# Kernel optimization log

Hardware: AMD Instinct MI355X
Metric: run time of the kernel (lower is better)

Reference implementation:

```python
import jax, jax.numpy as jnp
import numpy as np

TOP_K = 2

def setup_inputs() -> dict:
    key = jax.random.key(0)
    k0, k1, k2, k3 = jax.random.split(key, 4)
    B, S, D, F, E = 4, 4096, 1024, 2048, 8
    x = jax.random.normal(k0, (B, S, D), dtype=jnp.float32)
    w_router = jax.random.normal(k1, (E, D), dtype=jnp.float32) * 0.02
    w1 = jax.random.normal(k2, (E, F, D), dtype=jnp.float32) * 0.02
    w2 = jax.random.normal(k3, (E, D, F), dtype=jnp.float32) * 0.02
    return {"x": x, "w_router": w_router, "w1": w1, "w2": w2}

def reference(x, w_router, w1, w2):
    # x: [B,S,D]; w_router: [E,D]; w1: [E,F,D]; w2: [E,D,F]
    B, S, D = x.shape
    E = w_router.shape[0]
    xf = x.reshape(-1, D)                      # [T,D], T = B*S
    T = xf.shape[0]
    logits = xf @ w_router.T                   # [T,E]
    probs = jax.nn.softmax(logits, axis=-1)    # [T,E]
    top_v, top_i = jax.lax.top_k(probs, TOP_K) # [T,K]
    top_v = top_v / jnp.sum(top_v, axis=-1, keepdims=True)
    # dense combine weights: w[t,e] = renormalized prob if e in top-k else 0
    comb = jnp.zeros_like(probs).at[jnp.arange(T)[:, None], top_i].add(top_v)  # [T,E]
    # dense per-expert compute, masked/weighted combine (same math as gather-MLP-scatter;
    # dropout is identity in eval). GELU is exact (erf), matching torch F.gelu default.
    out = jnp.zeros_like(xf)
    for e in range(E):  # small fixed expert loop
        h = jax.nn.gelu(xf @ w1[e].T, approximate=False)   # [T,F]
        out = out + comb[:, e:e + 1] * (h @ w2[e].T)       # [T,D]
    expert_usage = jnp.mean(probs, axis=0)                  # [E]
    aux_loss = E * jnp.sum(expert_usage ** 2)
    return out.reshape(B, S, D), aux_loss
```

## Files before the change

### kernel.cpp

```cpp
#include <hip/hip_runtime.h>
#include <hip/hip_bf16.h>
#include <math.h>

typedef __attribute__((ext_vector_type(8))) short s16x8;
typedef __attribute__((ext_vector_type(4))) float f32x4;

#define T_TOK 16384
#define D_DIM 1024
#define F_DIM 2048
#define E_NUM 8
#define RCAP 34816

__device__ __forceinline__ unsigned short f2b(float f) {
  unsigned u = __float_as_uint(f);
  u += 0x7fff + ((u >> 16) & 1);
  return (unsigned short)(u >> 16);
}
__device__ __forceinline__ unsigned pk2(float a, float b) {
  __hip_bfloat162 h = __float22bfloat162_rn(make_float2(a, b));
  return *reinterpret_cast<unsigned*>(&h);
}

__global__ void castw_k(const float* __restrict__ w1, const float* __restrict__ w2,
                        unsigned short* __restrict__ w1b, unsigned short* __restrict__ w2b) {
  size_t i = ((size_t)blockIdx.x * 256 + threadIdx.x) * 4;
  float4 a = *(const float4*)(w1 + i);
  float4 b = *(const float4*)(w2 + i);
  uint2 ua, ub;
  ua.x = pk2(a.x, a.y); ua.y = pk2(a.z, a.w);
  ub.x = pk2(b.x, b.y); ub.y = pk2(b.z, b.w);
  *(uint2*)(w1b + i) = ua;
  *(uint2*)(w2b + i) = ub;
}

__global__ void router_k(const float* __restrict__ x, const float* __restrict__ wr,
                         int* __restrict__ topi, float* __restrict__ topw,
                         float* __restrict__ probs8, unsigned short* __restrict__ xb) {
  int tid = threadIdx.x, wid = tid >> 6, lane = tid & 63;
  int t = blockIdx.x * 4 + wid;
  const float* xr = x + (size_t)t * D_DIM;
  float4 xv[4];
#pragma unroll
  for (int i = 0; i < 4; ++i) xv[i] = *(const float4*)(xr + i * 256 + lane * 4);
#pragma unroll
  for (int i = 0; i < 4; ++i) {
    uint2 u; u.x = pk2(xv[i].x, xv[i].y); u.y = pk2(xv[i].z, xv[i].w);
    *(uint2*)(xb + (size_t)t * D_DIM + i * 256 + lane * 4) = u;
  }
  float logit[E_NUM];
#pragma unroll
  for (int e = 0; e < E_NUM; ++e) {
    const float* wrow = wr + e * D_DIM;
    float p = 0.f;
#pragma unroll
    for (int i = 0; i < 4; ++i) {
      float4 wv = *(const float4*)(wrow + i * 256 + lane * 4);
      p += xv[i].x * wv.x + xv[i].y * wv.y + xv[i].z * wv.z + xv[i].w * wv.w;
    }
    for (int s = 32; s; s >>= 1) p += __shfl_xor(p, s);
    logit[e] = p;
  }
  if (lane == 0) {
    float m = logit[0];
    for (int e = 1; e < E_NUM; ++e) m = fmaxf(m, logit[e]);
    float pr[E_NUM];
    float sum = 0.f;
    for (int e = 0; e < E_NUM; ++e) { pr[e] = expf(logit[e] - m); sum += pr[e]; }
    float inv = 1.f / sum;
    for (int e = 0; e < E_NUM; ++e) { pr[e] *= inv; probs8[t * 8 + e] = pr[e]; }
    int i0 = 0;
    for (int e = 1; e < E_NUM; ++e) if (pr[e] > pr[i0]) i0 = e;
    int i1 = (i0 == 0) ? 1 : 0;
    for (int e = 0; e < E_NUM; ++e) if (e != i0 && pr[e] > pr[i1]) i1 = e;
    float wsum = pr[i0] + pr[i1];
    topi[2 * t] = i0;  topi[2 * t + 1] = i1;
    topw[2 * t] = pr[i0] / wsum;  topw[2 * t + 1] = pr[i1] / wsum;
  }
}

__global__ void hist_k(const int* __restrict__ topi, const float* __restrict__ probs8,
                       int* __restrict__ cnt, float* __restrict__ usage) {
  __shared__ int sc[E_NUM];
  __shared__ float su[E_NUM];
  int tid = threadIdx.x;
  if (tid < E_NUM) { sc[tid] = 0; su[tid] = 0.f; }
  __syncthreads();
  for (int i = blockIdx.x * 256 + tid; i < 2 * T_TOK; i += 256 * 64)
    atomicAdd(&sc[topi[i]], 1);
  for (int i = blockIdx.x * 256 + tid; i < 8 * T_TOK; i += 256 * 64)
    atomicAdd(&su[i & 7], probs8[i]);
  __syncthreads();
  if (tid < E_NUM) { atomicAdd(&cnt[tid], sc[tid]); atomicAdd(&usage[tid], su[tid]); }
}

__global__ void scan_k(const int* __restrict__ cnt, int* __restrict__ offs,
                       const float* __restrict__ usage, float* __restrict__ aux) {
  if (threadIdx.x == 0 && blockIdx.x == 0) {
    int o = 0;
    for (int e = 0; e < E_NUM; ++e) { offs[e] = o; o += (cnt[e] + 255) & ~255; }
    offs[E_NUM] = o;
    float s = 0.f;
    for (int e = 0; e < E_NUM; ++e) { float m = usage[e] * (1.f / T_TOK); s += m * m; }
    *aux = (float)E_NUM * s;
  }
}

__global__ void assign_k(const int* __restrict__ topi, const int* __restrict__ offs,
                         int* __restrict__ cur, int* __restrict__ rowpair) {
  int p = blockIdx.x * 256 + threadIdx.x;
  int lane = threadIdx.x & 63;
  int e = topi[p];
  int r = 0;
#pragma unroll
  for (int ee = 0; ee < E_NUM; ++ee) {
    unsigned long long mask = __ballot(e == ee);
    if (e == ee) {
      int leader = __ffsll((unsigned long long)mask) - 1;
      int rank = __popcll(mask & ((1ull << lane) - 1ull));
      int b = 0;
      if (lane == leader) b = atomicAdd(&cur[ee], (int)__popcll(mask));
      b = __shfl(b, leader);
      r = offs[ee] + b + rank;
    }
  }
  rowpair[r] = p;
}


#define RGEMM_BODY(NT, EPILOGUE)                                               \
  f32x4 acc[4][4] = {};                                                        \
  s16x8 rA[4], rB[4];                                                          \
  _Pragma("unroll") for (int i = 0; i < 4; ++i) {                              \
    rA[i] = *(const s16x8*)(pA[i]);                                            \
    rB[i] = *(const s16x8*)(pB[i]);                                            \
  }                                                                            \
  _Pragma("unroll 2")                                                          \
  for (int t = 0; t < NT; ++t) {                                               \
    if (t) __syncthreads();                                                    \
    _Pragma("unroll") for (int i = 0; i < 4; ++i) {                            \
      *(s16x8*)&As[wo[i]] = rA[i];                                             \
      *(s16x8*)&Bs[wo[i]] = rB[i];                                             \
    }                                                                          \
    __syncthreads();                                                           \
    if (t < NT - 1) {                                                          \
      int k0 = (t + 1) * 64;                                                   \
      _Pragma("unroll") for (int i = 0; i < 4; ++i) {                          \
        rA[i] = *(const s16x8*)(pA[i] + k0);                                   \
        rB[i] = *(const s16x8*)(pB[i] + k0);                                   \
      }                                                                        \
    }                                                                          \
    int ar = wm * 64 + rl, br = wn * 64 + rl;                                  \
    _Pragma("unroll") for (int kk = 0; kk < 2; ++kk) {                         \
      int cs = (((kk * 4 + g4) ^ (rl & 7)) << 3);                              \
      s16x8 a[4], b[4];                                                        \
      _Pragma("unroll") for (int m = 0; m < 4; ++m)                            \
        a[m] = *(const s16x8*)&As[(ar + m * 16) * 64 + cs];                    \
      _Pragma("unroll") for (int n = 0; n < 4; ++n)                            \
        b[n] = *(const s16x8*)&Bs[(br + n * 16) * 64 + cs];                    \
      __builtin_amdgcn_s_setprio(1);                                           \
      _Pragma("unroll") for (int m = 0; m < 4; ++m)                            \
        _Pragma("unroll") for (int n = 0; n < 4; ++n)                          \
          acc[m][n] = __builtin_amdgcn_mfma_f32_16x16x32_bf16(                 \
              a[m], b[n], acc[m][n], 0, 0, 0);                                 \
      __builtin_amdgcn_s_setprio(0);                                           \
    }                                                                          \
  }                                                                            \
  EPILOGUE

__global__ __launch_bounds__(256, 3) void gemm1v_k(
    const unsigned short* __restrict__ xb, const unsigned short* __restrict__ w1b,
    const int* __restrict__ offs, const int* __restrict__ rowpair,
    const unsigned short* __restrict__ zrow,
    unsigned short* __restrict__ hseg, int segbase, int segrows) {
  int bid0 = blockIdx.x;
  int bid = ((bid0 & 7) << 11) | (bid0 >> 3);
  int e = bid >> 11, rem = bid & 2047, mt = rem >> 4, nt = rem & 15;
  int rend = offs[e + 1];
  int rowbase = offs[e] + mt * 128;
  if (rowbase >= rend || rowbase < segbase || rowbase >= segbase + segrows) return;

  __shared__ short As[128 * 64];
  __shared__ short Bs[128 * 64];
  int tid = threadIdx.x, wid = tid >> 6, lane = tid & 63;
  int wm = wid >> 1, wn = wid & 1, rl = lane & 15, g4 = lane >> 4;
  int j7 = tid & 7, rr = tid >> 3;
  int wg = ((j7 ^ (rr & 7)) << 3);
  int wo[4];
#pragma unroll
  for (int i = 0; i < 4; ++i) wo[i] = (rr + i * 32) * 64 + wg;

  const unsigned short* pA[4];
  const unsigned short* pB[4];
#pragma unroll
  for (int i = 0; i < 4; ++i) {
    int p = rowpair[rowbase + rr + i * 32];
    pA[i] = (p >= 0 ? xb + (size_t)(p >> 1) * D_DIM : zrow) + j7 * 8;
    pB[i] = w1b + ((size_t)e * F_DIM + nt * 128 + rr + i * 32) * D_DIM + j7 * 8;
  }

  RGEMM_BODY(16, {
    size_t rloc = (size_t)(rowbase - segbase);
    int c0 = nt * 128 + wn * 64 + rl;
    int lr0 = wm * 64 + (g4 << 2);
    _Pragma("unroll") for (int m = 0; m < 4; ++m)
      _Pragma("unroll") for (int j = 0; j < 4; ++j) {
        size_t rrow = (rloc + lr0 + m * 16 + j) * F_DIM;
        _Pragma("unroll") for (int n = 0; n < 4; ++n) {
          float v = acc[m][n][j];
          float g = 0.5f * v * (1.f + erff(v * 0.70710678118f));
          hseg[rrow + c0 + n * 16] = f2b(g);
        }
      }
  })
}

__global__ __launch_bounds__(256, 3) void gemm2v_k(
    const unsigned short* __restrict__ hseg, const unsigned short* __restrict__ w2b,
    const int* __restrict__ offs, const int* __restrict__ rowpair,
    const float* __restrict__ topw, float* __restrict__ out,
    int segbase, int segrows) {
  int bid0 = blockIdx.x;
  int bid = ((bid0 & 7) << 10) | (bid0 >> 3);
  int e = bid >> 10, rem = bid & 1023, mt = rem >> 3, nt = rem & 7;
  int rend = offs[e + 1];
  int rowbase = offs[e] + mt * 128;
  if (rowbase >= rend || rowbase < segbase || rowbase >= segbase + segrows) return;

  __shared__ short As[128 * 64];
  __shared__ short Bs[128 * 64];
  int tid = threadIdx.x, wid = tid >> 6, lane = tid & 63;
  int wm = wid >> 1, wn = wid & 1, rl = lane & 15, g4 = lane >> 4;
  int j7 = tid & 7, rr = tid >> 3;
  int wg = ((j7 ^ (rr & 7)) << 3);
  int wo[4];
#pragma unroll
  for (int i = 0; i < 4; ++i) wo[i] = (rr + i * 32) * 64 + wg;

  size_t rloc = (size_t)(rowbase - segbase);
  const unsigned short* pA[4];
  const unsigned short* pB[4];
#pragma unroll
  for (int i = 0; i < 4; ++i) {
    pA[i] = hseg + (rloc + rr + i * 32) * F_DIM + j7 * 8;
    pB[i] = w2b + ((size_t)e * D_DIM + nt * 128 + rr + i * 32) * F_DIM + j7 * 8;
  }

  RGEMM_BODY(32, {
    int c0 = nt * 128 + wn * 64 + rl;
    int lr0 = wm * 64 + (g4 << 2);
    _Pragma("unroll") for (int m = 0; m < 4; ++m)
      _Pragma("unroll") for (int j = 0; j < 4; ++j) {
        int lr = lr0 + m * 16 + j;
        int p = rowpair[rowbase + lr];
        if (p >= 0) {
          float wgt = topw[p];
          float* op = out + (size_t)(p >> 1) * D_DIM + c0;
          _Pragma("unroll") for (int n = 0; n < 4; ++n)
            unsafeAtomicAdd(op + n * 16, wgt * acc[m][n][j]);
        }
      }
  })
}

extern "C" void kernel_launch(void* const* d_in, const int* in_sizes, int n_in,
                              void* d_out, int out_size, void* d_ws, size_t ws_size,
                              hipStream_t stream) {
  const float* x  = (const float*)d_in[0];
  const float* wr = (const float*)d_in[1];
  const float* w1 = (const float*)d_in[2];
  const float* w2 = (const float*)d_in[3];
  float* out = (float*)d_out;

  char* ws = (char*)d_ws;
  int* cnt   = (int*)ws;
  int* cur   = cnt + 8;
  int* offs  = cnt + 16;
  float* usage = (float*)(cnt + 25);
  unsigned short* zrow = (unsigned short*)(ws + 4096);
  size_t off = 8192;
  int*   topi = (int*)(ws + off);     off += (size_t)2 * T_TOK * 4;
  float* topw = (float*)(ws + off);   off += (size_t)2 * T_TOK * 4;
  int*   rowpair = (int*)(ws + off);  off += (size_t)RCAP * 4;
  float* probs8 = (float*)(ws + off); off += (size_t)T_TOK * 8 * 4;
  off = (off + 255) & ~(size_t)255;

  unsigned short* xb = (unsigned short*)(ws + off);
  off += (size_t)T_TOK * D_DIM * 2;
  unsigned short* w1b = (unsigned short*)(ws + off);
  off += (size_t)E_NUM * F_DIM * D_DIM * 2;
  unsigned short* w2b = (unsigned short*)(ws + off);
  off += (size_t)E_NUM * F_DIM * D_DIM * 2;
  if (ws_size < off + (size_t)4096 * F_DIM * 2) return;
  size_t avail = ws_size - off;
  size_t segcap = (avail / ((size_t)F_DIM * 2)) & ~(size_t)255;
  int segrows = segcap > (size_t)RCAP ? RCAP : (int)segcap;
  unsigned short* hseg = (unsigned short*)(ws + off);
  int nseg = (RCAP + segrows - 1) / segrows;

  hipMemsetAsync(ws, 0, 8192, stream);
  hipMemsetAsync(rowpair, 0xFF, (size_t)RCAP * 4, stream);
  hipMemsetAsync(d_out, 0, (size_t)out_size * 4, stream);
  castw_k<<<16384, 256, 0, stream>>>(w1, w2, w1b, w2b);
  router_k<<<T_TOK / 4, 256, 0, stream>>>(x, wr, topi, topw, probs8, xb);
  hist_k<<<64, 256, 0, stream>>>(topi, probs8, cnt, usage);
  scan_k<<<1, 64, 0, stream>>>(cnt, offs, usage, out + (size_t)T_TOK * D_DIM);
  assign_k<<<2 * T_TOK / 256, 256, 0, stream>>>(topi, offs, cur, rowpair);

  for (int s = 0; s < nseg; ++s) {
    int segbase = s * segrows;
    gemm1v_k<<<16384, 256, 0, stream>>>(xb, w1b, offs, rowpair, zrow, hseg, segbase, segrows);
    gemm2v_k<<<8192, 256, 0, stream>>>(hseg, w2b, offs, rowpair, topw, out, segbase, segrows);
  }
}
```

Before: 571.7 us.

## Double-buffer GEMM LDS tiles and replace atomic scatter with store-then-combine

Gives the shared GEMM body two LDS buffers so each k-step writes the next tile into the other buffer, removing one barrier per iteration. Launch bounds drop from 3 to 2 blocks per CU to fit the larger shared-memory footprint. When the workspace is large enough, the second GEMM writes bf16 per-slot outputs to a buffer instead of doing float atomics into the output. A new combine kernel then gathers each token's two slots, weights them and writes the output, which also removes the output memset. The cost is an extra bf16 rounding of the expert outputs, lower occupancy, and an extra pass over a large intermediate buffer.

```diff
diff --git a/kernel.cpp b/kernel.cpp
--- a/kernel.cpp
+++ b/kernel.cpp
@@ -15,6 +15,9 @@
   unsigned u = __float_as_uint(f);
   u += 0x7fff + ((u >> 16) & 1);
   return (unsigned short)(u >> 16);
+}
+__device__ __forceinline__ float b2f(unsigned short h) {
+  return __uint_as_float(((unsigned)h) << 16);
 }
 __device__ __forceinline__ unsigned pk2(float a, float b) {
   __hip_bfloat162 h = __float22bfloat162_rn(make_float2(a, b));
@@ -106,7 +109,8 @@
 }
 
 __global__ void assign_k(const int* __restrict__ topi, const int* __restrict__ offs,
-                         int* __restrict__ cur, int* __restrict__ rowpair) {
+                         int* __restrict__ cur, int* __restrict__ rowpair,
+                         int* __restrict__ pos) {
   int p = blockIdx.x * 256 + threadIdx.x;
   int lane = threadIdx.x & 63;
   int e = topi[p];
@@ -124,6 +128,7 @@
     }
   }
   rowpair[r] = p;
+  pos[p] = r;
 }
 
 
@@ -136,10 +141,11 @@
   }                                                                            \
   _Pragma("unroll 2")                                                          \
   for (int t = 0; t < NT; ++t) {                                               \
-    if (t) __syncthreads();                                                    \
+    short* Asw = As[t & 1];                                                    \
+    short* Bsw = Bs[t & 1];                                                    \
     _Pragma("unroll") for (int i = 0; i < 4; ++i) {                            \
-      *(s16x8*)&As[wo[i]] = rA[i];                                             \
-      *(s16x8*)&Bs[wo[i]] = rB[i];                                             \
+      *(s16x8*)&Asw[wo[i]] = rA[i];                                            \
+      *(s16x8*)&Bsw[wo[i]] = rB[i];                                            \
     }                                                                          \
     __syncthreads();                                                           \
     if (t < NT - 1) {                                                          \
@@ -154,9 +160,9 @@
       int cs = (((kk * 4 + g4) ^ (rl & 7)) << 3);                              \
       s16x8 a[4], b[4];                                                        \
       _Pragma("unroll") for (int m = 0; m < 4; ++m)                            \
-        a[m] = *(const s16x8*)&As[(ar + m * 16) * 64 + cs];                    \
+        a[m] = *(const s16x8*)&Asw[(ar + m * 16) * 64 + cs];                   \
       _Pragma("unroll") for (int n = 0; n < 4; ++n)                            \
-        b[n] = *(const s16x8*)&Bs[(br + n * 16) * 64 + cs];                    \
+        b[n] = *(const s16x8*)&Bsw[(br + n * 16) * 64 + cs];                   \
       __builtin_amdgcn_s_setprio(1);                                           \
       _Pragma("unroll") for (int m = 0; m < 4; ++m)                            \
         _Pragma("unroll") for (int n = 0; n < 4; ++n)                          \
@@ -167,7 +173,7 @@
   }                                                                            \
   EPILOGUE
 
-__global__ __launch_bounds__(256, 3) void gemm1v_k(
+__global__ __launch_bounds__(256, 2) void gemm1v_k(
     const unsigned short* __restrict__ xb, const unsigned short* __restrict__ w1b,
     const int* __restrict__ offs, const int* __restrict__ rowpair,
     const unsigned short* __restrict__ zrow,
@@ -179,8 +185,8 @@
   int rowbase = offs[e] + mt * 128;
   if (rowbase >= rend || rowbase < segbase || rowbase >= segbase + segrows) return;
 
-  __shared__ short As[128 * 64];
-  __shared__ short Bs[128 * 64];
+  __shared__ short As[2][128 * 64];
+  __shared__ short Bs[2][128 * 64];
   int tid = threadIdx.x, wid = tid >> 6, lane = tid & 63;
   int wm = wid >> 1, wn = wid & 1, rl = lane & 15, g4 = lane >> 4;
   int j7 = tid & 7, rr = tid >> 3;
@@ -214,7 +220,49 @@
   })
 }
 
-__global__ __launch_bounds__(256, 3) void gemm2v_k(
+__global__ __launch_bounds__(256, 2) void gemm2s_k(
+    const unsigned short* __restrict__ hseg, const unsigned short* __restrict__ w2b,
+    const int* __restrict__ offs, unsigned short* __restrict__ obuf,
+    int segbase, int segrows) {
+  int bid0 = blockIdx.x;
+  int bid = ((bid0 & 7) << 10) | (bid0 >> 3);
+  int e = bid >> 10, rem = bid & 1023, mt = rem >> 3, nt = rem & 7;
+  int rend = offs[e + 1];
+  int rowbase = offs[e] + mt * 128;
+  if (rowbase >= rend || rowbase < segbase || rowbase >= segbase + segrows) return;
+
+  __shared__ short As[2][128 * 64];
+  __shared__ short Bs[2][128 * 64];
+  int tid = threadIdx.x, wid = tid >> 6, lane = tid & 63;
+  int wm = wid >> 1, wn = wid & 1, rl = lane & 15, g4 = lane >> 4;
+  int j7 = tid & 7, rr = tid >> 3;
+  int wg = ((j7 ^ (rr & 7)) << 3);
+  int wo[4];
+#pragma unroll
+  for (int i = 0; i < 4; ++i) wo[i] = (rr + i * 32) * 64 + wg;
+
+  size_t rloc = (size_t)(rowbase - segbase);
+  const unsigned short* pA[4];
+  const unsigned short* pB[4];
+#pragma unroll
+  for (int i = 0; i < 4; ++i) {
+    pA[i] = hseg + (rloc + rr + i * 32) * F_DIM + j7 * 8;
+    pB[i] = w2b + ((size_t)e * D_DIM + nt * 128 + rr + i * 32) * F_DIM + j7 * 8;
+  }
+
+  RGEMM_BODY(32, {
+    int c0 = nt * 128 + wn * 64 + rl;
+    int lr0 = wm * 64 + (g4 << 2);
+    _Pragma("unroll") for (int m = 0; m < 4; ++m)
+      _Pragma("unroll") for (int j = 0; j < 4; ++j) {
+        size_t rrow = (size_t)(rowbase + lr0 + m * 16 + j) * D_DIM;
+        _Pragma("unroll") for (int n = 0; n < 4; ++n)
+          obuf[rrow + c0 + n * 16] = f2b(acc[m][n][j]);
+      }
+  })
+}
+
+__global__ __launch_bounds__(256, 2) void gemm2v_k(
     const unsigned short* __restrict__ hseg, const unsigned short* __restrict__ w2b,
     const int* __restrict__ offs, const int* __restrict__ rowpair,
     const float* __restrict__ topw, float* __restrict__ out,
@@ -226,8 +274,8 @@
   int rowbase = offs[e] + mt * 128;
   if (rowbase >= rend || rowbase < segbase || rowbase >= segbase + segrows) return;
 
-  __shared__ short As[128 * 64];
-  __shared__ short Bs[128 * 64];
+  __shared__ short As[2][128 * 64];
+  __shared__ short Bs[2][128 * 64];
   int tid = threadIdx.x, wid = tid >> 6, lane = tid & 63;
   int wm = wid >> 1, wn = wid & 1, rl = lane & 15, g4 = lane >> 4;
   int j7 = tid & 7, rr = tid >> 3;
@@ -262,6 +310,26 @@
   })
 }
 
+__global__ void combine_k(const unsigned short* __restrict__ obuf, const int* __restrict__ pos,
+                          const float* __restrict__ topw, float* __restrict__ out) {
+  int u = blockIdx.x * 256 + threadIdx.x;
+  int t = u >> 7;
+  int d0 = (u & 127) * 8;
+  int p0 = pos[2 * t], p1 = pos[2 * t + 1];
+  float w0 = topw[2 * t], w1 = topw[2 * t + 1];
+  s16x8 a = *(const s16x8*)(obuf + (size_t)p0 * D_DIM + d0);
+  s16x8 b = *(const s16x8*)(obuf + (size_t)p1 * D_DIM + d0);
+  float r[8];
+#pragma unroll
+  for (int j = 0; j < 8; ++j)
+    r[j] = w0 * b2f((unsigned short)a[j]) + w1 * b2f((unsigned short)b[j]);
+  float4 lo = {r[0], r[1], r[2], r[3]};
+  float4 hi = {r[4], r[5], r[6], r[7]};
+  float* o = out + (size_t)t * D_DIM + d0;
+  *(float4*)o = lo;
+  *(float4*)(o + 4) = hi;
+}
+
 extern "C" void kernel_launch(void* const* d_in, const int* in_sizes, int n_in,
                               void* d_out, int out_size, void* d_ws, size_t ws_size,
                               hipStream_t stream) {
@@ -281,6 +349,7 @@
   int*   topi = (int*)(ws + off);     off += (size_t)2 * T_TOK * 4;
   float* topw = (float*)(ws + off);   off += (size_t)2 * T_TOK * 4;
   int*   rowpair = (int*)(ws + off);  off += (size_t)RCAP * 4;
+  int*   pos = (int*)(ws + off);      off += (size_t)2 * T_TOK * 4;
   float* probs8 = (float*)(ws + off); off += (size_t)T_TOK * 8 * 4;
   off = (off + 255) & ~(size_t)255;
 
@@ -290,7 +359,16 @@
   off += (size_t)E_NUM * F_DIM * D_DIM * 2;
   unsigned short* w2b = (unsigned short*)(ws + off);
   off += (size_t)E_NUM * F_DIM * D_DIM * 2;
-  if (ws_size < off + (size_t)4096 * F_DIM * 2) return;
+
+  const size_t obytes = (size_t)RCAP * D_DIM * 2;
+  const size_t minseg = (size_t)4096 * F_DIM * 2;
+  bool storepath = false;
+  unsigned short* obuf = nullptr;
+  if (ws_size >= off + obytes + minseg) {
+    storepath = true;
+    obuf = (unsigned short*)(ws + off); off += obytes;
+  }
+  if (ws_size < off + minseg) return;
   size_t avail = ws_size - off;
   size_t segcap = (avail / ((size_t)F_DIM * 2)) & ~(size_t)255;
   int segrows = segcap > (size_t)RCAP ? RCAP : (int)segcap;
@@ -299,16 +377,21 @@
 
   hipMemsetAsync(ws, 0, 8192, stream);
   hipMemsetAsync(rowpair, 0xFF, (size_t)RCAP * 4, stream);
-  hipMemsetAsync(d_out, 0, (size_t)out_size * 4, stream);
+  if (!storepath) hipMemsetAsync(d_out, 0, (size_t)out_size * 4, stream);
   castw_k<<<16384, 256, 0, stream>>>(w1, w2, w1b, w2b);
   router_k<<<T_TOK / 4, 256, 0, stream>>>(x, wr, topi, topw, probs8, xb);
   hist_k<<<64, 256, 0, stream>>>(topi, probs8, cnt, usage);
   scan_k<<<1, 64, 0, stream>>>(cnt, offs, usage, out + (size_t)T_TOK * D_DIM);
-  assign_k<<<2 * T_TOK / 256, 256, 0, stream>>>(topi, offs, cur, rowpair);
+  assign_k<<<2 * T_TOK / 256, 256, 0, stream>>>(topi, offs, cur, rowpair, pos);
 
   for (int s = 0; s < nseg; ++s) {
     int segbase = s * segrows;
     gemm1v_k<<<16384, 256, 0, stream>>>(xb, w1b, offs, rowpair, zrow, hseg, segbase, segrows);
-    gemm2v_k<<<8192, 256, 0, stream>>>(hseg, w2b, offs, rowpair, topw, out, segbase, segrows);
-  }
-}
+    if (storepath)
+      gemm2s_k<<<8192, 256, 0, stream>>>(hseg, w2b, offs, obuf, segbase, segrows);
+    else
+      gemm2v_k<<<8192, 256, 0, stream>>>(hseg, w2b, offs, rowpair, topw, out, segbase, segrows);
+  }
+  if (storepath)
+    combine_k<<<T_TOK * D_DIM / 8 / 256, 256, 0, stream>>>(obuf, pos, topw, out);
+}
```

Result: slower. 857.2 us (+49.9%).
